# Optimization experiments

Measured on AMD Instinct MI355X. Metric: run time of the kernel, lower is better.

Reference implementation:

```python
import jax, jax.numpy as jnp
import numpy as np

DELTA = 0.1

def setup_inputs() -> dict:
    key = jax.random.key(0)
    k1, k2 = jax.random.split(key)
    B, T_text, adim, T_feats = 16, 512, 256, 4096
    hs = jax.random.normal(k1, (B, T_text, adim), dtype=jnp.float32)
    ds = jax.random.randint(k2, (B, T_text), 0, 16, dtype=jnp.int32)
    h_masks = jnp.ones((B, T_feats), dtype=bool)
    d_masks = jnp.ones((B, T_text), dtype=bool)
    return {"hs": hs, "ds": ds, "h_masks": h_masks, "d_masks": d_masks}


def reference(hs, ds, h_masks, d_masks):
    # hs: (B, T_text, adim), ds: (B, T_text), h_masks: (B, T_feats), d_masks: (B, T_text)
    B, T_feats = h_masks.shape
    ds_f = ds.astype(jnp.float32)
    # frame time indices, zeroed where h_mask is False
    t = jnp.arange(T_feats, dtype=jnp.float32)[None, :] * h_masks.astype(jnp.float32)  # (B, T_feats)
    # Gaussian centers per token
    c = jnp.cumsum(ds_f, axis=-1) - ds_f / 2.0  # (B, T_text)
    # energy: (B, T_feats, T_text)
    energy = -DELTA * (t[:, :, None] - c[:, None, :]) ** 2
    energy = jnp.where(d_masks[:, None, :], energy, -jnp.inf)
    p_attn = jax.nn.softmax(energy, axis=2)
    # weighted sum over text tokens -> (B, T_feats, adim)
    return jnp.einsum('btl,bld->btd', p_attn, hs)
```

## Files before the change

### kernel.cpp

```cpp
#include <hip/hip_runtime.h>
#include <math.h>

#define BATCH   16
#define T_TEXT  512
#define ADIM    256
#define T_FEATS 4096
#define DELTA   0.1f
#define WF      8
#define NW      4
#define TFB     (WF * NW)
#define MAXW    64
#define WPAD    68

typedef float f32x4 __attribute__((ext_vector_type(4)));

__global__ __launch_bounds__(T_TEXT) void centers_kernel(
    const int* __restrict__ ds, float* __restrict__ c_out)
{
    __shared__ float s[T_TEXT];
    const int b = blockIdx.x;
    const int l = threadIdx.x;
    const float v = (float)ds[b * T_TEXT + l];
    s[l] = v;
    for (int off = 1; off < T_TEXT; off <<= 1) {
        __syncthreads();
        float x = (l >= off) ? s[l - off] : 0.0f;
        __syncthreads();
        s[l] += x;
    }
    __syncthreads();
    c_out[b * T_TEXT + l] = s[l] - 0.5f * v;
}

__global__ __launch_bounds__(256) void gauss_upsample_kernel(
    const float* __restrict__ hs, const float* __restrict__ c_g,
    float* __restrict__ out)
{
    __shared__ float cs[T_TEXT];
    __shared__ float W[NW][WF][WPAD];
    __shared__ float shsw[NW][WF];

    const int tilesPerB = T_FEATS / TFB;
    const int b    = blockIdx.x / tilesPerB;
    const int tile = blockIdx.x % tilesPerB;
    const int tid  = threadIdx.x;
    const int g    = tid >> 6;
    const int ln   = tid & 63;

    cs[tid]       = c_g[b * T_TEXT + tid];
    cs[tid + 256] = c_g[b * T_TEXT + tid + 256];
    __syncthreads();

    const int   fw0 = tile * TFB + g * WF;
    const float tw  = (float)fw0;
    const int   fq  = ln >> 3;
    const float t   = tw + (float)fq;

    int lo = 0, sp = 64;
    #pragma unroll
    for (int r = 0; r < 3; ++r) {
        const int   p  = lo - 1 + ((ln & 7) + 1) * sp;
        const float cv = cs[p < T_TEXT ? p : T_TEXT - 1];
        const bool  pr = (p < T_TEXT) && (cv < t);
        const unsigned long long mk = __ballot(pr);
        const int c = __popcll((mk >> (8 * fq)) & 0xffULL);
        lo += c * sp;
        sp >>= 3;
    }

    float dmin = 1e30f;
    if (lo < T_TEXT) dmin = cs[lo] - t;
    if (lo > 0)      dmin = fminf(dmin, t - cs[lo - 1]);
    const float m  = -DELTA * dmin * dmin;
    const float Rw = sqrtf(fmaf(dmin, dmin, 270.0f));

    const int   bq  = (ln >> 2) & 1;
    const int   qj  = (ln & 3) + 1;
    const float tgt = bq ? (t + Rw) : (t - Rw);
    int alo = 0, sq = 128;
    #pragma unroll
    for (int r = 0; r < 4; ++r) {
        const int   p  = alo - 1 + qj * sq;
        const float cv = cs[p < T_TEXT ? p : T_TEXT - 1];
        const bool  pr = (p < T_TEXT) && (bq ? (cv <= tgt) : (cv < tgt));
        const unsigned long long mk = __ballot(pr);
        const int c = __popcll((mk >> (ln & 60)) & 0xfULL);
        alo += c * sq;
        sq >>= 2;
    }
    {
        const int   p  = alo - 1 + qj;
        const float cv = cs[p < T_TEXT ? p : T_TEXT - 1];
        const bool  pr = (p < T_TEXT) && (bq ? (cv <= tgt) : (cv < tgt));
        const unsigned long long mk = __ballot(pr);
        const int c = __popcll((mk >> (ln & 60)) & 0xfULL);
        alo += c;
    }

    int vmin = bq ? 0x7fffffff : alo;
    int vmax = bq ? alo : -1;
    #pragma unroll
    for (int off = 1; off < 64; off <<= 1) {
        vmin = min(vmin, __shfl_xor(vmin, off, 64));
        vmax = max(vmax, __shfl_xor(vmax, off, 64));
    }
    const int L0 = vmin, L1 = vmax;

    float mreg[WF];
    #pragma unroll
    for (int k = 0; k < WF; ++k) mreg[k] = __shfl(m, 8 * k, 64);

    if (ln < WF) shsw[g][ln] = 0.0f;

    const float* __restrict__ hsb = hs + (size_t)b * T_TEXT * ADIM;

    float4 acc[WF];
    #pragma unroll
    for (int fl = 0; fl < WF; ++fl) acc[fl] = make_float4(0.f, 0.f, 0.f, 0.f);

    for (int cb = L0; cb < L1; cb += MAXW) {
        const int cn = min(MAXW, L1 - cb);

        const float cj = (ln < cn) ? cs[cb + ln] : 0.0f;
        #pragma unroll
        for (int k = 0; k < WF; ++k) {
            float w = 0.0f;
            if (ln < cn) {
                const float dd = (tw + (float)k) - cj;
                w = __expf(fmaf(-DELTA * dd, dd, -mreg[k]));
            }
            W[g][k][ln] = w;
        }

        {
            const int rf = ln >> 3, rg = ln & 7;
            float s = 0.0f;
            #pragma unroll
            for (int k = 0; k < 8; ++k) s += W[g][rf][rg + 8 * k];
            s += __shfl_xor(s, 1, 64);
            s += __shfl_xor(s, 2, 64);
            s += __shfl_xor(s, 4, 64);
            if (rg == 0) shsw[g][rf] += s;
        }

        for (int jb = cb; jb < cb + cn; jb += 4) {
            const int col = jb - cb;
            const int r0 = jb;
            const int r1 = min(jb + 1, T_TEXT - 1);
            const int r2 = min(jb + 2, T_TEXT - 1);
            const int r3 = min(jb + 3, T_TEXT - 1);
            const float4 h0 = ((const float4*)(hsb + (size_t)r0 * ADIM))[ln];
            const float4 h1 = ((const float4*)(hsb + (size_t)r1 * ADIM))[ln];
            const float4 h2 = ((const float4*)(hsb + (size_t)r2 * ADIM))[ln];
            const float4 h3 = ((const float4*)(hsb + (size_t)r3 * ADIM))[ln];
            #pragma unroll
            for (int fl = 0; fl < WF; ++fl) {
                const float4 w4 = *((const float4*)&W[g][fl][col]);
                acc[fl].x = fmaf(w4.x, h0.x, acc[fl].x);
                acc[fl].y = fmaf(w4.x, h0.y, acc[fl].y);
                acc[fl].z = fmaf(w4.x, h0.z, acc[fl].z);
                acc[fl].w = fmaf(w4.x, h0.w, acc[fl].w);
                acc[fl].x = fmaf(w4.y, h1.x, acc[fl].x);
                acc[fl].y = fmaf(w4.y, h1.y, acc[fl].y);
                acc[fl].z = fmaf(w4.y, h1.z, acc[fl].z);
                acc[fl].w = fmaf(w4.y, h1.w, acc[fl].w);
                acc[fl].x = fmaf(w4.z, h2.x, acc[fl].x);
                acc[fl].y = fmaf(w4.z, h2.y, acc[fl].y);
                acc[fl].z = fmaf(w4.z, h2.z, acc[fl].z);
                acc[fl].w = fmaf(w4.z, h2.w, acc[fl].w);
                acc[fl].x = fmaf(w4.w, h3.x, acc[fl].x);
                acc[fl].y = fmaf(w4.w, h3.y, acc[fl].y);
                acc[fl].z = fmaf(w4.w, h3.z, acc[fl].z);
                acc[fl].w = fmaf(w4.w, h3.w, acc[fl].w);
            }
        }
    }

    float* __restrict__ outb = out + ((size_t)b * T_FEATS + (size_t)fw0) * ADIM;
    #pragma unroll
    for (int fl = 0; fl < WF; ++fl) {
        const float inv = 1.0f / shsw[g][fl];
        f32x4 o;
        o.x = acc[fl].x * inv; o.y = acc[fl].y * inv;
        o.z = acc[fl].z * inv; o.w = acc[fl].w * inv;
        __builtin_nontemporal_store(o, ((f32x4*)(outb + (size_t)fl * ADIM)) + ln);
    }
}

extern "C" void kernel_launch(void* const* d_in, const int* in_sizes, int n_in,
                              void* d_out, int out_size, void* d_ws, size_t ws_size,
                              hipStream_t stream)
{
    const float* hs = (const float*)d_in[0];
    const int*   ds = (const int*)d_in[1];
    float* out  = (float*)d_out;
    float* c_ws = (float*)d_ws;

    centers_kernel<<<BATCH, T_TEXT, 0, stream>>>(ds, c_ws);

    const int blocks = BATCH * (T_FEATS / TFB);
    gauss_upsample_kernel<<<blocks, 256, 0, stream>>>(hs, c_ws, out);
}
```

Before: 24.63 us.

## Split each wave's 8 frames into two halves with tighter token windows

Each wavefront now handles its eight frames in two passes of four, and each pass computes its own token-range bounds from half-wave reductions. The aim is to narrow the band of text tokens whose weights and hs rows are processed per pass, cutting wasted exp and FMA work, and to halve the accumulator registers. In exchange, hs rows in the overlap of the two windows are loaded twice and the loop overhead runs twice.

```diff
diff --git a/kernel.cpp b/kernel.cpp
--- a/kernel.cpp
+++ b/kernel.cpp
@@ -37,7 +37,7 @@
     float* __restrict__ out)
 {
     __shared__ float cs[T_TEXT];
-    __shared__ float W[NW][WF][WPAD];
+    __shared__ float W[NW][4][WPAD];
     __shared__ float shsw[NW][WF];
 
     const int tilesPerB = T_FEATS / TFB;
@@ -97,93 +97,106 @@
         alo += c;
     }
 
-    int vmin = bq ? 0x7fffffff : alo;
-    int vmax = bq ? alo : -1;
-    #pragma unroll
-    for (int off = 1; off < 64; off <<= 1) {
-        vmin = min(vmin, __shfl_xor(vmin, off, 64));
-        vmax = max(vmax, __shfl_xor(vmax, off, 64));
-    }
-    const int L0 = vmin, L1 = vmax;
+    int hmin = bq ? 0x7fffffff : alo;
+    int hmax = bq ? alo : -1;
+    #pragma unroll
+    for (int off = 1; off < 32; off <<= 1) {
+        hmin = min(hmin, __shfl_xor(hmin, off, 32));
+        hmax = max(hmax, __shfl_xor(hmax, off, 32));
+    }
+    const int oMin = __shfl_xor(hmin, 32, 64);
+    const int oMax = __shfl_xor(hmax, 32, 64);
+    const int L0_0 = (ln < 32) ? hmin : oMin;
+    const int L1_0 = (ln < 32) ? hmax : oMax;
+    const int L0_1 = (ln < 32) ? oMin : hmin;
+    const int L1_1 = (ln < 32) ? oMax : hmax;
 
     float mreg[WF];
     #pragma unroll
     for (int k = 0; k < WF; ++k) mreg[k] = __shfl(m, 8 * k, 64);
 
-    if (ln < WF) shsw[g][ln] = 0.0f;
-
     const float* __restrict__ hsb = hs + (size_t)b * T_TEXT * ADIM;
-
-    float4 acc[WF];
-    #pragma unroll
-    for (int fl = 0; fl < WF; ++fl) acc[fl] = make_float4(0.f, 0.f, 0.f, 0.f);
-
-    for (int cb = L0; cb < L1; cb += MAXW) {
-        const int cn = min(MAXW, L1 - cb);
-
-        const float cj = (ln < cn) ? cs[cb + ln] : 0.0f;
+    float* __restrict__ outb = out + ((size_t)b * T_FEATS + (size_t)fw0) * ADIM;
+
+    #pragma unroll
+    for (int h = 0; h < 2; ++h) {
+        const int P0 = h ? L0_1 : L0_0;
+        const int P1 = h ? L1_1 : L1_0;
+
+        if (ln < 4) shsw[g][4 * h + ln] = 0.0f;
+
+        float4 acc[4];
         #pragma unroll
-        for (int k = 0; k < WF; ++k) {
-            float w = 0.0f;
-            if (ln < cn) {
-                const float dd = (tw + (float)k) - cj;
-                w = __expf(fmaf(-DELTA * dd, dd, -mreg[k]));
+        for (int fl = 0; fl < 4; ++fl) acc[fl] = make_float4(0.f, 0.f, 0.f, 0.f);
+
+        for (int cb = P0; cb < P1; cb += MAXW) {
+            const int cn = min(MAXW, P1 - cb);
+
+            const float cj = (ln < cn) ? cs[cb + ln] : 0.0f;
+            #pragma unroll
+            for (int k = 0; k < 4; ++k) {
+                const int row = 4 * h + k;
+                float w = 0.0f;
+                if (ln < cn) {
+                    const float dd = (tw + (float)row) - cj;
+                    w = __expf(fmaf(-DELTA * dd, dd, -mreg[row]));
+                }
+                W[g][k][ln] = w;
             }
-            W[g][k][ln] = w;
-        }
-
-        {
-            const int rf = ln >> 3, rg = ln & 7;
-            float s = 0.0f;
-            #pragma unroll
-            for (int k = 0; k < 8; ++k) s += W[g][rf][rg + 8 * k];
-            s += __shfl_xor(s, 1, 64);
-            s += __shfl_xor(s, 2, 64);
-            s += __shfl_xor(s, 4, 64);
-            if (rg == 0) shsw[g][rf] += s;
-        }
-
-        for (int jb = cb; jb < cb + cn; jb += 4) {
-            const int col = jb - cb;
-            const int r0 = jb;
-            const int r1 = min(jb + 1, T_TEXT - 1);
-            const int r2 = min(jb + 2, T_TEXT - 1);
-            const int r3 = min(jb + 3, T_TEXT - 1);
-            const float4 h0 = ((const float4*)(hsb + (size_t)r0 * ADIM))[ln];
-            const float4 h1 = ((const float4*)(hsb + (size_t)r1 * ADIM))[ln];
-            const float4 h2 = ((const float4*)(hsb + (size_t)r2 * ADIM))[ln];
-            const float4 h3 = ((const float4*)(hsb + (size_t)r3 * ADIM))[ln];
-            #pragma unroll
-            for (int fl = 0; fl < WF; ++fl) {
-                const float4 w4 = *((const float4*)&W[g][fl][col]);
-                acc[fl].x = fmaf(w4.x, h0.x, acc[fl].x);
-                acc[fl].y = fmaf(w4.x, h0.y, acc[fl].y);
-                acc[fl].z = fmaf(w4.x, h0.z, acc[fl].z);
-                acc[fl].w = fmaf(w4.x, h0.w, acc[fl].w);
-                acc[fl].x = fmaf(w4.y, h1.x, acc[fl].x);
-                acc[fl].y = fmaf(w4.y, h1.y, acc[fl].y);
-                acc[fl].z = fmaf(w4.y, h1.z, acc[fl].z);
-                acc[fl].w = fmaf(w4.y, h1.w, acc[fl].w);
-                acc[fl].x = fmaf(w4.z, h2.x, acc[fl].x);
-                acc[fl].y = fmaf(w4.z, h2.y, acc[fl].y);
-                acc[fl].z = fmaf(w4.z, h2.z, acc[fl].z);
-                acc[fl].w = fmaf(w4.z, h2.w, acc[fl].w);
-                acc[fl].x = fmaf(w4.w, h3.x, acc[fl].x);
-                acc[fl].y = fmaf(w4.w, h3.y, acc[fl].y);
-                acc[fl].z = fmaf(w4.w, h3.z, acc[fl].z);
-                acc[fl].w = fmaf(w4.w, h3.w, acc[fl].w);
+
+            {
+                const int rf = ln >> 4, rg = ln & 15;
+                float s = W[g][rf][rg] + W[g][rf][rg + 16]
+                        + W[g][rf][rg + 32] + W[g][rf][rg + 48];
+                s += __shfl_xor(s, 1, 64);
+                s += __shfl_xor(s, 2, 64);
+                s += __shfl_xor(s, 4, 64);
+                s += __shfl_xor(s, 8, 64);
+                if (rg == 0) shsw[g][4 * h + rf] += s;
+            }
+
+            for (int jb = cb; jb < cb + cn; jb += 4) {
+                const int col = jb - cb;
+                const int r0 = jb;
+                const int r1 = min(jb + 1, T_TEXT - 1);
+                const int r2 = min(jb + 2, T_TEXT - 1);
+                const int r3 = min(jb + 3, T_TEXT - 1);
+                const float4 h0 = ((const float4*)(hsb + (size_t)r0 * ADIM))[ln];
+                const float4 h1 = ((const float4*)(hsb + (size_t)r1 * ADIM))[ln];
+                const float4 h2 = ((const float4*)(hsb + (size_t)r2 * ADIM))[ln];
+                const float4 h3 = ((const float4*)(hsb + (size_t)r3 * ADIM))[ln];
+                #pragma unroll
+                for (int fl = 0; fl < 4; ++fl) {
+                    const float4 w4 = *((const float4*)&W[g][fl][col]);
+                    acc[fl].x = fmaf(w4.x, h0.x, acc[fl].x);
+                    acc[fl].y = fmaf(w4.x, h0.y, acc[fl].y);
+                    acc[fl].z = fmaf(w4.x, h0.z, acc[fl].z);
+                    acc[fl].w = fmaf(w4.x, h0.w, acc[fl].w);
+                    acc[fl].x = fmaf(w4.y, h1.x, acc[fl].x);
+                    acc[fl].y = fmaf(w4.y, h1.y, acc[fl].y);
+                    acc[fl].z = fmaf(w4.y, h1.z, acc[fl].z);
+                    acc[fl].w = fmaf(w4.y, h1.w, acc[fl].w);
+                    acc[fl].x = fmaf(w4.z, h2.x, acc[fl].x);
+                    acc[fl].y = fmaf(w4.z, h2.y, acc[fl].y);
+                    acc[fl].z = fmaf(w4.z, h2.z, acc[fl].z);
+                    acc[fl].w = fmaf(w4.z, h2.w, acc[fl].w);
+                    acc[fl].x = fmaf(w4.w, h3.x, acc[fl].x);
+                    acc[fl].y = fmaf(w4.w, h3.y, acc[fl].y);
+                    acc[fl].z = fmaf(w4.w, h3.z, acc[fl].z);
+                    acc[fl].w = fmaf(w4.w, h3.w, acc[fl].w);
+                }
             }
         }
-    }
-
-    float* __restrict__ outb = out + ((size_t)b * T_FEATS + (size_t)fw0) * ADIM;
-    #pragma unroll
-    for (int fl = 0; fl < WF; ++fl) {
-        const float inv = 1.0f / shsw[g][fl];
-        f32x4 o;
-        o.x = acc[fl].x * inv; o.y = acc[fl].y * inv;
-        o.z = acc[fl].z * inv; o.w = acc[fl].w * inv;
-        __builtin_nontemporal_store(o, ((f32x4*)(outb + (size_t)fl * ADIM)) + ln);
+
+        #pragma unroll
+        for (int fl = 0; fl < 4; ++fl) {
+            const float inv = 1.0f / shsw[g][4 * h + fl];
+            f32x4 o;
+            o.x = acc[fl].x * inv; o.y = acc[fl].y * inv;
+            o.z = acc[fl].z * inv; o.w = acc[fl].w * inv;
+            __builtin_nontemporal_store(o,
+                ((f32x4*)(outb + (size_t)(4 * h + fl) * ADIM)) + ln);
+        }
     }
 }
 
```

Result: slower. 25.51 us (+3.5%).
